# Performance work log

Hardware: AMD Instinct MI355X
Metric: run time of the kernel (lower is better)

Reference implementation:

```python
import jax, jax.numpy as jnp
import numpy as np

B, P, NOBJ = 16, 19248, 32
NUM_CLASSES = 81  # 80 foreground + background (code uses num_classes+1 w/o focal loss)
POS_TH, NEG_TH = 0.5, 0.4
VAR0, VAR1 = 0.1, 0.2  # standard SSD encode variances
NEGPOS_RATIO = 3


def setup_inputs() -> dict:
    key = jax.random.key(0)
    k1, k2, k3, k4, k5 = jax.random.split(key, 5)
    loc_data = jax.random.normal(k1, (B, P, 4), jnp.float32)
    conf_data = jax.random.normal(k2, (B, P, NUM_CLASSES), jnp.float32)
    # priors in (cx, cy, w, h), normalized coords
    pc = jax.random.uniform(k3, (P, 2), jnp.float32, 0.05, 0.95)
    pw = jax.random.uniform(jax.random.fold_in(k3, 1), (P, 2), jnp.float32, 0.05, 0.4)
    priors = jnp.concatenate([pc, pw], -1)
    # gt boxes in point form (xmin, ymin, xmax, ymax)
    gc = jax.random.uniform(k4, (B, NOBJ, 2), jnp.float32, 0.2, 0.8)
    gw = jax.random.uniform(jax.random.fold_in(k4, 1), (B, NOBJ, 2), jnp.float32, 0.05, 0.3)
    gt_boxes = jnp.concatenate([gc - gw / 2, gc + gw / 2], -1)
    gt_labels = jax.random.randint(k5, (B, NOBJ), 0, NUM_CLASSES - 1)  # 0..79
    return {"loc_data": loc_data, "conf_data": conf_data, "priors": priors,
            "gt_boxes": gt_boxes, "gt_labels": gt_labels}


def _point_form(p):
    # (cx,cy,w,h) -> (xmin,ymin,xmax,ymax)
    return jnp.concatenate([p[..., :2] - p[..., 2:] / 2, p[..., :2] + p[..., 2:] / 2], -1)


def _jaccard(a, b):
    # a: [N,4], b: [P,4] point form -> IoU [N,P]
    lt = jnp.maximum(a[:, None, :2], b[None, :, :2])
    rb = jnp.minimum(a[:, None, 2:], b[None, :, 2:])
    wh = jnp.clip(rb - lt, 0.0)
    inter = wh[..., 0] * wh[..., 1]
    area_a = (a[:, 2] - a[:, 0]) * (a[:, 3] - a[:, 1])
    area_b = (b[:, 2] - b[:, 0]) * (b[:, 3] - b[:, 1])
    return inter / (area_a[:, None] + area_b[None, :] - inter)


def _match_one(gt, labels, priors_pf, priors):
    # SSD match: per-prior best gt + force each gt's best prior to be positive
    ov = _jaccard(gt, priors_pf)                 # [N,P]
    best_prior_idx = jnp.argmax(ov, axis=1)      # [N]
    best_truth_ov = jnp.max(ov, axis=0)          # [P]
    best_truth_idx = jnp.argmax(ov, axis=0)      # [P]
    best_truth_ov = best_truth_ov.at[best_prior_idx].set(2.0)
    best_truth_idx = best_truth_idx.at[best_prior_idx].set(jnp.arange(gt.shape[0]))
    matched = gt[best_truth_idx]                 # [P,4] point form
    conf = labels[best_truth_idx] + 1
    conf = jnp.where(best_truth_ov < POS_TH, -1, conf)   # neutral band
    conf = jnp.where(best_truth_ov < NEG_TH, 0, conf)    # background
    # encode offsets with variances
    m_cxcy = (matched[:, :2] + matched[:, 2:]) / 2
    m_wh = matched[:, 2:] - matched[:, :2]
    g_cxcy = (m_cxcy - priors[:, :2]) / (VAR0 * priors[:, 2:])
    g_wh = jnp.log(m_wh / priors[:, 2:]) / VAR1
    return jnp.concatenate([g_cxcy, g_wh], -1), conf


def reference(loc_data, conf_data, priors, gt_boxes, gt_labels):
    priors_pf = _point_form(priors)
    loc_t, conf_t = jax.vmap(lambda g, l: _match_one(g, l, priors_pf, priors))(gt_boxes, gt_labels)
    loc_t = jax.lax.stop_gradient(loc_t)
    pos = conf_t > 0                                   # [B,P]
    n_pos = pos.sum(axis=1)                            # [B]
    N = jnp.maximum(pos.sum(), 1).astype(loc_data.dtype)
    # localization: smooth L1 over positives
    d = loc_data - loc_t
    ad = jnp.abs(d)
    sl1 = jnp.where(ad < 1.0, 0.5 * d * d, ad - 0.5)
    loss_l = jnp.sum(sl1 * pos[..., None])
    # confidence: hard negative mining at 3:1
    logp = jax.nn.log_softmax(conf_data, axis=-1)      # [B,P,C]
    ct = jnp.maximum(conf_t, 0)
    nll = -jnp.take_along_axis(logp, ct[..., None], axis=-1)[..., 0]  # [B,P]
    mine = jnp.where(pos | (conf_t < 0), 0.0, nll)     # exclude pos & neutral from mining
    rank = jnp.argsort(jnp.argsort(-mine, axis=1), axis=1)
    num_neg = jnp.minimum(NEGPOS_RATIO * n_pos, P - 1)
    neg = (rank < num_neg[:, None]) & (conf_t == 0)
    loss_c = jnp.sum(nll * (pos | neg))
    return jnp.stack([loss_l, loss_c]) / N
```

## Files before the change

### kernel.cpp

```cpp
#include <hip/hip_runtime.h>
#include <cstdint>
#include <cstddef>

#define BB 16
#define PP 19248
#define NOBJ 32
#define NCLS 81
#define POS_TH 0.5f
#define NEG_TH 0.4f
#define VAR0 0.1f
#define VAR1 0.2f
#define NEGPOS 3

#define MTB 256
#define NMB ((PP + MTB - 1) / MTB)
#define MAINB 1024
#define ROWS_PB 64
#define NSLOT ((PP + ROWS_PB - 1) / ROWS_PB)
#define NSLOTW (NSLOT * 16)
#define ST 1024

#define MCH 8
#define CHLEN (PP / MCH)
#define MJOBS (BB * NOBJ * MCH)
#define MBLK (MJOBS / 4)

#define HSHIFT 19
#define HSIZE 8192
#define HPT (HSIZE / ST)
#define CAP HSIZE

__global__ __launch_bounds__(MTB) void k_match(const float* __restrict__ priors,
                                               const float* __restrict__ gt_boxes,
                                               unsigned long long* __restrict__ gkey) {
    const int wid = threadIdx.x >> 6, lane = threadIdx.x & 63;
    const int job = blockIdx.x * 4 + wid;
    const int b = job >> 8;
    const int n = (job >> 3) & 31;
    const int c = job & 7;

    const float4 g = ((const float4*)gt_boxes)[b * NOBJ + n];
    float garea;
    {
#pragma clang fp contract(off)
        garea = (g.z - g.x) * (g.w - g.y);
    }

    unsigned long long bestkey = 0ull;
    const int pbeg = c * CHLEN;
    const int pend = pbeg + CHLEN;
    for (int p = pbeg + lane; p < pend; p += 64) {
        float4 pr = ((const float4*)priors)[p];
        float iou;
        {
#pragma clang fp contract(off)
            float hw = pr.z / 2.0f, hh = pr.w / 2.0f;
            float px1 = pr.x - hw, py1 = pr.y - hh, px2 = pr.x + hw, py2 = pr.y + hh;
            float parea = (px2 - px1) * (py2 - py1);
            float ix1 = fmaxf(g.x, px1), iy1 = fmaxf(g.y, py1);
            float ix2 = fminf(g.z, px2), iy2 = fminf(g.w, py2);
            float iw = fmaxf(ix2 - ix1, 0.0f), ih = fmaxf(iy2 - iy1, 0.0f);
            float inter = iw * ih;
            iou = inter / (garea + parea - inter);
        }
        unsigned long long key = (((unsigned long long)__float_as_uint(iou)) << 32) |
                                 (unsigned long long)(0xFFFFFFFFu - (unsigned)p);
        if (key > bestkey) bestkey = key;
    }
#pragma unroll
    for (int m = 1; m < 64; m <<= 1) {
        unsigned long long o = __shfl_xor(bestkey, m, 64);
        if (o > bestkey) bestkey = o;
    }
    if (lane == 0) atomicMax(&gkey[b * NOBJ + n], bestkey);
}

__global__ __launch_bounds__(MTB) void k_prior(const float* __restrict__ priors,
                                               const float* __restrict__ gt_boxes,
                                               int* __restrict__ bp) {
    const int b = blockIdx.y;
    const int p = blockIdx.x * MTB + threadIdx.x;
    __shared__ float4 sg[NOBJ];
    if (threadIdx.x < NOBJ) sg[threadIdx.x] = ((const float4*)gt_boxes)[b * NOBJ + threadIdx.x];
    __syncthreads();
    if (p >= PP) return;

    float4 pr = ((const float4*)priors)[p];
    float px1, py1, px2, py2, parea;
    {
#pragma clang fp contract(off)
        float hw = pr.z / 2.0f, hh = pr.w / 2.0f;
        px1 = pr.x - hw; py1 = pr.y - hh; px2 = pr.x + hw; py2 = pr.y + hh;
        parea = (px2 - px1) * (py2 - py1);
    }

    float best = -1.0f;
    int bn = 0;
#pragma unroll 4
    for (int n = 0; n < NOBJ; ++n) {
        float4 g = sg[n];
        float iou;
        {
#pragma clang fp contract(off)
            float ix1 = fmaxf(g.x, px1), iy1 = fmaxf(g.y, py1);
            float ix2 = fminf(g.z, px2), iy2 = fminf(g.w, py2);
            float iw = fmaxf(ix2 - ix1, 0.0f), ih = fmaxf(iy2 - iy1, 0.0f);
            float inter = iw * ih;
            float garea = (g.z - g.x) * (g.w - g.y);
            iou = inter / (garea + parea - inter);
        }
        if (iou > best) { best = iou; bn = n; }
    }
    int cls = 2;
    if (best < POS_TH) cls = 1;
    if (best < NEG_TH) cls = 0;
    bp[(size_t)b * PP + p] = (bn << 2) | cls;
}

__device__ __forceinline__ float sl1(float d) {
    float ad = fabsf(d);
    return ad < 1.0f ? 0.5f * d * d : ad - 0.5f;
}

__global__ __launch_bounds__(MAINB) void k_main(const float* __restrict__ loc_data,
                                                const float* __restrict__ conf_data,
                                                const float* __restrict__ priors,
                                                const float* __restrict__ gt_boxes,
                                                const int* __restrict__ gt_labels,
                                                const int* __restrict__ bp,
                                                const unsigned long long* __restrict__ gkey,
                                                float* __restrict__ mine,
                                                float* __restrict__ p_ll,
                                                float* __restrict__ p_lc,
                                                int* __restrict__ p_np) {
    const int b = blockIdx.y;
    const int t = threadIdx.x;
    const int wid = t >> 6;
    const int lane = t & 63;
    const int g = lane >> 4;
    const int j = lane & 15;
    const int rbase = blockIdx.x * ROWS_PB + wid * 4;
    const int r = rbase + g;
    const bool valid = r < PP;
    const int slot = blockIdx.x * 16 + wid;

    unsigned pst = 0xFFFFFFFFu;
    int labreg = 0;
    if (lane < NOBJ) {
        pst = 0xFFFFFFFFu - (unsigned)(gkey[b * NOBJ + lane] & 0xFFFFFFFFull);
        labreg = gt_labels[b * NOBJ + lane];
    }

    const float* rowp = conf_data + ((size_t)b * PP + r) * NCLS;
    float c0 = 0.f, c1 = 0.f, c2 = 0.f, c3 = 0.f, c4 = 0.f, c80 = 0.f;
    int packed = 0;
    if (valid) {
        c0 = rowp[j];
        c1 = rowp[j + 16];
        c2 = rowp[j + 32];
        c3 = rowp[j + 48];
        c4 = rowp[j + 64];
        if (j == 0) c80 = rowp[80];
        packed = bp[(size_t)b * PP + r];
    }

    float s = __expf(c0) + __expf(c1) + __expf(c2) + __expf(c3) + __expf(c4);
    if (j == 0) s += __expf(c80);
    s += __shfl_xor(s, 1, 64);
    s += __shfl_xor(s, 2, 64);
    s += __shfl_xor(s, 4, 64);
    s += __shfl_xor(s, 8, 64);
    const float lse = __logf(s);

    unsigned long long b0 = __ballot(pst == (unsigned)(rbase + 0));
    unsigned long long b1 = __ballot(pst == (unsigned)(rbase + 1));
    unsigned long long b2 = __ballot(pst == (unsigned)(rbase + 2));
    unsigned long long b3 = __ballot(pst == (unsigned)(rbase + 3));
    unsigned long long mball = (g == 0) ? b0 : (g == 1) ? b1 : (g == 2) ? b2 : b3;

    int ti = packed >> 2;
    int cls = packed & 3;
    if (mball) { ti = 63 - __builtin_clzll(mball); cls = 2; }

    const int lab = __shfl(labreg, ti, 64);
    int conf_c = (cls == 2) ? (lab + 1) : ((cls == 1) ? -1 : 0);

    const float row0 = __shfl(c0, lane & 48, 64);
    const float nll0 = lse - row0;

    float my_ll = 0.0f, my_lc = 0.0f;
    int my_pos = 0;

    if (valid && j == 0) {
        mine[(size_t)b * PP + r] = (conf_c == 0) ? nll0 : 0.0f;
        if (conf_c > 0) {
            my_pos = 1;
            my_lc = lse - rowp[conf_c];
            float4 gbox = ((const float4*)gt_boxes)[b * NOBJ + ti];
            float4 pr = ((const float4*)priors)[r];
            float mcx = (gbox.x + gbox.z) / 2.0f, mcy = (gbox.y + gbox.w) / 2.0f;
            float mw = gbox.z - gbox.x, mh = gbox.w - gbox.y;
            float t0 = (mcx - pr.x) / (VAR0 * pr.z);
            float t1 = (mcy - pr.y) / (VAR0 * pr.w);
            float t2 = logf(mw / pr.z) / VAR1;
            float t3 = logf(mh / pr.w) / VAR1;
            float4 ld = ((const float4*)loc_data)[(size_t)b * PP + r];
            my_ll = sl1(ld.x - t0) + sl1(ld.y - t1) + sl1(ld.z - t2) + sl1(ld.w - t3);
        }
    }

    if (__ballot(my_pos != 0) == 0ull) {
        if (lane == 0) {
            p_ll[b * NSLOTW + slot] = 0.0f;
            p_lc[b * NSLOTW + slot] = 0.0f;
            p_np[b * NSLOTW + slot] = 0;
        }
    } else {
        for (int off = 32; off > 0; off >>= 1) {
            my_ll += __shfl_down(my_ll, off, 64);
            my_lc += __shfl_down(my_lc, off, 64);
            my_pos += __shfl_down(my_pos, off, 64);
        }
        if (lane == 0) {
            p_ll[b * NSLOTW + slot] = my_ll;
            p_lc[b * NSLOTW + slot] = my_lc;
            p_np[b * NSLOTW + slot] = my_pos;
        }
    }
}

__global__ __launch_bounds__(ST) void k_select(const float* __restrict__ mine,
                                               const float* __restrict__ p_ll,
                                               const float* __restrict__ p_lc,
                                               const int* __restrict__ p_np,
                                               float* __restrict__ acc,
                                               int* __restrict__ acc_np,
                                               unsigned* __restrict__ done,
                                               float* __restrict__ out) {
    const int b = blockIdx.x;
    const int tid = threadIdx.x;
    const int wid = tid >> 6, lane = tid & 63;
    constexpr int NW = ST / 64;

    __shared__ unsigned hist[HSIZE];
    __shared__ unsigned s_tsum[ST];
    __shared__ unsigned s_wsum[NW];
    __shared__ float rll[NW], rlc[NW];
    __shared__ int rnp[NW];
    __shared__ float rs1[NW], rs2[NW];
    __shared__ unsigned rc2[NW];
    __shared__ float s_ll, s_lc, s_neg;
    __shared__ int s_np, s_B, s_G1;
    __shared__ unsigned s_cntB, s_cnt, s_prefix;
    __shared__ int s_rem;
    __shared__ unsigned h16[16];
    __shared__ unsigned swh[NW * 16];
    __shared__ unsigned stot[16];

    float ll = 0.0f, lc = 0.0f;
    int np = 0;
    for (int i = tid; i < NSLOTW; i += ST) {
        ll += p_ll[b * NSLOTW + i];
        lc += p_lc[b * NSLOTW + i];
        np += p_np[b * NSLOTW + i];
    }
    for (int off = 32; off > 0; off >>= 1) {
        ll += __shfl_down(ll, off, 64);
        lc += __shfl_down(lc, off, 64);
        np += __shfl_down(np, off, 64);
    }
    if (lane == 0) { rll[wid] = ll; rlc[wid] = lc; rnp[wid] = np; }
    __syncthreads();
    if (tid == 0) {
        float a = 0.0f, c = 0.0f;
        int n = 0;
        for (int w = 0; w < NW; ++w) { a += rll[w]; c += rlc[w]; n += rnp[w]; }
        s_ll = a; s_lc = c; s_np = n;
        s_neg = 0.0f;
    }
    __syncthreads();
    const int np_b = s_np;
    const int k = min(NEGPOS * np_b, PP - 1);

    const float* mv = mine + (size_t)b * PP;
    const float4* mv4 = (const float4*)mv;
    constexpr int PP4 = PP / 4;

    if (k > 0) {
        for (int i = tid; i < HSIZE; i += ST) hist[i] = 0u;
        __syncthreads();
        for (int i = tid; i < PP4; i += ST) {
            float4 v = mv4[i];
            atomicAdd(&hist[__float_as_uint(v.x) >> HSHIFT], 1u);
            atomicAdd(&hist[__float_as_uint(v.y) >> HSHIFT], 1u);
            atomicAdd(&hist[__float_as_uint(v.z) >> HSHIFT], 1u);
            atomicAdd(&hist[__float_as_uint(v.w) >> HSHIFT], 1u);
        }
        __syncthreads();

        unsigned tsum = 0;
        const int hb = tid * HPT;
#pragma unroll
        for (int v = 0; v < HPT; ++v) tsum += hist[hb + v];
        s_tsum[tid] = tsum;
        unsigned wsum = tsum;
        for (int off = 32; off > 0; off >>= 1) wsum += __shfl_down(wsum, off, 64);
        if (lane == 0) s_wsum[wid] = wsum;
        __syncthreads();
        if (tid == 0) {
            unsigned cum = 0;
            int w = NW - 1;
            for (; w > 0; --w) {
                if (cum + s_wsum[w] >= (unsigned)k) break;
                cum += s_wsum[w];
            }
            int t = (w + 1) * 64 - 1;
            for (; t > w * 64; --t) {
                if (cum + s_tsum[t] >= (unsigned)k) break;
                cum += s_tsum[t];
            }
            int bin = t * HPT + HPT - 1;
            for (; bin > t * HPT; --bin) {
                if (cum + hist[bin] >= (unsigned)k) break;
                cum += hist[bin];
            }
            s_B = bin;
            s_G1 = (int)cum;
            s_cntB = hist[bin];
            s_cnt = 0u;
        }
        __syncthreads();
        const int B = s_B;
        const int r = k - s_G1;
        const unsigned cntB = s_cntB;
        const unsigned bin_lo = (unsigned)B << HSHIFT;
        const unsigned hi_base = (unsigned)(B + 1) << HSHIFT;
        unsigned* cbuf = hist;

        if (cntB <= CAP) {
            float S1 = 0.0f;
            for (int i = tid; i < PP4; i += ST) {
                float4 v = mv4[i];
                unsigned bx = __float_as_uint(v.x);
                unsigned by = __float_as_uint(v.y);
                unsigned bz = __float_as_uint(v.z);
                unsigned bw = __float_as_uint(v.w);
                if (bx >= hi_base) S1 += v.x;
                else if (bx >= bin_lo) cbuf[atomicAdd(&s_cnt, 1u)] = bx;
                if (by >= hi_base) S1 += v.y;
                else if (by >= bin_lo) cbuf[atomicAdd(&s_cnt, 1u)] = by;
                if (bz >= hi_base) S1 += v.z;
                else if (bz >= bin_lo) cbuf[atomicAdd(&s_cnt, 1u)] = bz;
                if (bw >= hi_base) S1 += v.w;
                else if (bw >= bin_lo) cbuf[atomicAdd(&s_cnt, 1u)] = bw;
            }
            for (int off = 32; off > 0; off >>= 1) S1 += __shfl_down(S1, off, 64);
            if (lane == 0) rs1[wid] = S1;
            __syncthreads();

            if (tid == 0) { s_prefix = bin_lo; s_rem = r; }
            __syncthreads();
            for (int pass = 0; pass < 5; ++pass) {
                const int shift = (pass < 4) ? (15 - 4 * pass) : 0;
                const int width = (pass < 4) ? 4 : 3;
                const int nb = 1 << width;
                const unsigned hm = 0xFFFFFFFFu << (shift + width);
                if (tid < 16) h16[tid] = 0u;
                __syncthreads();
                const unsigned prefix = s_prefix;
                for (unsigned i = tid; i < cntB; i += ST) {
                    unsigned bits = cbuf[i];
                    if ((bits & hm) == prefix)
                        atomicAdd(&h16[(bits >> shift) & (nb - 1)], 1u);
                }
                __syncthreads();
                if (tid == 0) {
                    int rem = s_rem;
                    unsigned cum = 0;
                    int chosen = 0;
                    for (int v = nb - 1; v >= 0; --v) {
                        unsigned c = h16[v];
                        if (cum + c >= (unsigned)rem) { chosen = v; s_rem = rem - (int)cum; break; }
                        cum += c;
                    }
                    s_prefix = prefix | ((unsigned)chosen << shift);
                }
                __syncthreads();
            }
            const unsigned T = s_prefix;

            float S2 = 0.0f;
            unsigned c2 = 0;
            for (unsigned i = tid; i < cntB; i += ST) {
                unsigned bits = cbuf[i];
                if (bits > T) { S2 += __uint_as_float(bits); c2++; }
            }
            for (int off = 32; off > 0; off >>= 1) {
                S2 += __shfl_down(S2, off, 64);
                c2 += __shfl_down(c2, off, 64);
            }
            if (lane == 0) { rs2[wid] = S2; rc2[wid] = c2; }
            __syncthreads();
            if (tid == 0) {
                float S1t = 0.0f, S2t = 0.0f;
                unsigned c2t = 0;
                for (int w = 0; w < NW; ++w) { S1t += rs1[w]; S2t += rs2[w]; c2t += rc2[w]; }
                s_neg = S1t + S2t + (float)(r - (int)c2t) * __uint_as_float(T);
            }
            __syncthreads();
        } else {
            if (tid == 0) { s_prefix = 0u; s_rem = k; }
            __syncthreads();
            for (int pass = 0; pass < 8; ++pass) {
                const int shift = 28 - 4 * pass;
                const unsigned hm = (pass == 0) ? 0u : (0xFFFFFFFFu << (shift + 4));
                const unsigned prefix = s_prefix;
                unsigned cnt[16];
#pragma unroll
                for (int v = 0; v < 16; ++v) cnt[v] = 0u;
                for (int i = tid; i < PP; i += ST) {
                    unsigned bits = __float_as_uint(mv[i]);
                    unsigned key = ((bits & hm) == prefix) ? ((bits >> shift) & 15u) : 16u;
                    if (__any(key != 16u)) {
#pragma unroll
                        for (int v = 0; v < 16; ++v)
                            cnt[v] += (unsigned)__popcll(__ballot(key == (unsigned)v));
                    }
                }
                if (lane == 0) {
#pragma unroll
                    for (int v = 0; v < 16; ++v) swh[wid * 16 + v] = cnt[v];
                }
                __syncthreads();
                if (tid < 16) {
                    unsigned tt = 0;
#pragma unroll
                    for (int w = 0; w < NW; ++w) tt += swh[w * 16 + tid];
                    stot[tid] = tt;
                }
                __syncthreads();
                if (tid == 0) {
                    int rem = s_rem;
                    unsigned cum = 0;
                    int chosen = 0;
                    for (int v = 15; v >= 0; --v) {
                        unsigned c = stot[v];
                        if (cum + c >= (unsigned)rem) { chosen = v; s_rem = rem - (int)cum; break; }
                        cum += c;
                    }
                    s_prefix = prefix | ((unsigned)chosen << shift);
                }
                __syncthreads();
            }
            const unsigned T = s_prefix;
            float sum = 0.0f;
            unsigned cnt = 0;
            for (int i = tid; i < PP; i += ST) {
                float v = mv[i];
                if (__float_as_uint(v) > T) { sum += v; cnt++; }
            }
            for (int off = 32; off > 0; off >>= 1) {
                sum += __shfl_down(sum, off, 64);
                cnt += __shfl_down(cnt, off, 64);
            }
            if (lane == 0) { rs2[wid] = sum; rc2[wid] = cnt; }
            __syncthreads();
            if (tid == 0) {
                float S = 0.0f;
                int G = 0;
                for (int w = 0; w < NW; ++w) { S += rs2[w]; G += (int)rc2[w]; }
                s_neg = S + (float)(k - G) * __uint_as_float(T);
            }
            __syncthreads();
        }
    }

    if (tid == 0) {
        atomicAdd(&acc[0], s_ll);
        atomicAdd(&acc[1], s_lc + s_neg);
        atomicAdd(acc_np, np_b);
        __threadfence();
        unsigned prev = atomicAdd(done, 1u);
        if (prev == BB - 1) {
            int tp = atomicAdd(acc_np, 0);
            float N = (float)max(tp, 1);
            float a0 = atomicAdd(&acc[0], 0.0f);
            float a1 = atomicAdd(&acc[1], 0.0f);
            out[0] = a0 / N;
            out[1] = a1 / N;
        }
    }
}

extern "C" void kernel_launch(void* const* d_in, const int* in_sizes, int n_in,
                              void* d_out, int out_size, void* d_ws, size_t ws_size,
                              hipStream_t stream) {
    const float* loc    = (const float*)d_in[0];
    const float* conf   = (const float*)d_in[1];
    const float* priors = (const float*)d_in[2];
    const float* gt     = (const float*)d_in[3];
    const int*   labels = (const int*)d_in[4];
    float* out = (float*)d_out;

    char* ws = (char*)d_ws;
    const size_t SZ_BP = (size_t)BB * PP * 4;
    const size_t SZ_SLOT = (size_t)BB * NSLOTW * 4;
    unsigned long long* gkey = (unsigned long long*)ws;
    float*    acc    = (float*)   (ws + 4096);
    int*      acc_np = (int*)     (ws + 4104);
    unsigned* done   = (unsigned*)(ws + 4108);
    int*   bp   = (int*)  (ws + 4224);
    float* mine = (float*)(ws + 4224 + SZ_BP);
    float* p_ll = (float*)(ws + 4224 + 2 * SZ_BP);
    float* p_lc = (float*)(ws + 4224 + 2 * SZ_BP + SZ_SLOT);
    int*   p_np = (int*)  (ws + 4224 + 2 * SZ_BP + 2 * SZ_SLOT);

    (void)hipMemsetAsync(ws, 0, 4224, stream);

    k_match<<<MBLK, MTB, 0, stream>>>(priors, gt, gkey);

    dim3 pg(NMB, BB);
    k_prior<<<pg, MTB, 0, stream>>>(priors, gt, bp);

    dim3 kg(NSLOT, BB);
    k_main<<<kg, MAINB, 0, stream>>>(loc, conf, priors, gt, labels, bp, gkey,
                                     mine, p_ll, p_lc, p_np);

    k_select<<<BB, ST, 0, stream>>>(mine, p_ll, p_lc, p_np, acc, acc_np, done, out);
}
```

Before: 213.6 us.

## Apply forced matches in separate kernel and pack labels into prior map

Moves forced best-prior assignment out of k_main into a small k_force kernel that atomically overwrites the per-prior packed word, and has k_prior store the final label code directly. k_main no longer loads gkey/labels, runs four ballots, or shuffles the label per row. It also now processes 8 rows per wave with 8 lanes each (10 loads per lane), which halves the number of k_main blocks. The cost is an extra kernel launch plus serialized atomics. The packed-word encoding must preserve the priority of forced matches, with the largest n winning ties.

```diff
diff --git a/kernel.cpp b/kernel.cpp
--- a/kernel.cpp
+++ b/kernel.cpp
@@ -15,7 +15,7 @@
 #define MTB 256
 #define NMB ((PP + MTB - 1) / MTB)
 #define MAINB 1024
-#define ROWS_PB 64
+#define ROWS_PB 128
 #define NSLOT ((PP + ROWS_PB - 1) / ROWS_PB)
 #define NSLOTW (NSLOT * 16)
 #define ST 1024
@@ -77,11 +77,16 @@
 
 __global__ __launch_bounds__(MTB) void k_prior(const float* __restrict__ priors,
                                                const float* __restrict__ gt_boxes,
-                                               int* __restrict__ bp) {
+                                               const int* __restrict__ gt_labels,
+                                               unsigned* __restrict__ bp) {
     const int b = blockIdx.y;
     const int p = blockIdx.x * MTB + threadIdx.x;
     __shared__ float4 sg[NOBJ];
-    if (threadIdx.x < NOBJ) sg[threadIdx.x] = ((const float4*)gt_boxes)[b * NOBJ + threadIdx.x];
+    __shared__ int slab[NOBJ];
+    if (threadIdx.x < NOBJ) {
+        sg[threadIdx.x] = ((const float4*)gt_boxes)[b * NOBJ + threadIdx.x];
+        slab[threadIdx.x] = gt_labels[b * NOBJ + threadIdx.x];
+    }
     __syncthreads();
     if (p >= PP) return;
 
@@ -111,10 +116,23 @@
         }
         if (iou > best) { best = iou; bn = n; }
     }
-    int cls = 2;
-    if (best < POS_TH) cls = 1;
-    if (best < NEG_TH) cls = 0;
-    bp[(size_t)b * PP + p] = (bn << 2) | cls;
+    unsigned cc;
+    if (best < NEG_TH) cc = 1u;
+    else if (best < POS_TH) cc = 0u;
+    else cc = (unsigned)(slab[bn] + 2);
+    bp[(size_t)b * PP + p] = ((unsigned)bn << 8) | cc;
+}
+
+__global__ __launch_bounds__(512) void k_force(const int* __restrict__ gt_labels,
+                                               const unsigned long long* __restrict__ gkey,
+                                               unsigned* __restrict__ bp) {
+    const int i = threadIdx.x;
+    const int b = i >> 5, n = i & 31;
+    unsigned long long key = gkey[b * NOBJ + n];
+    unsigned pstar = 0xFFFFFFFFu - (unsigned)(key & 0xFFFFFFFFull);
+    int lab = gt_labels[b * NOBJ + n];
+    unsigned val = 0x80000000u | ((unsigned)n << 8) | (unsigned)(lab + 2);
+    atomicMax(&bp[(size_t)b * PP + pstar], val);
 }
 
 __device__ __forceinline__ float sl1(float d) {
@@ -126,9 +144,7 @@
                                                 const float* __restrict__ conf_data,
                                                 const float* __restrict__ priors,
                                                 const float* __restrict__ gt_boxes,
-                                                const int* __restrict__ gt_labels,
-                                                const int* __restrict__ bp,
-                                                const unsigned long long* __restrict__ gkey,
+                                                const unsigned* __restrict__ bp,
                                                 float* __restrict__ mine,
                                                 float* __restrict__ p_ll,
                                                 float* __restrict__ p_lc,
@@ -137,65 +153,46 @@
     const int t = threadIdx.x;
     const int wid = t >> 6;
     const int lane = t & 63;
-    const int g = lane >> 4;
-    const int j = lane & 15;
-    const int rbase = blockIdx.x * ROWS_PB + wid * 4;
+    const int g = lane >> 3;
+    const int j = lane & 7;
+    const int rbase = blockIdx.x * ROWS_PB + wid * 8;
     const int r = rbase + g;
     const bool valid = r < PP;
     const int slot = blockIdx.x * 16 + wid;
 
-    unsigned pst = 0xFFFFFFFFu;
-    int labreg = 0;
-    if (lane < NOBJ) {
-        pst = 0xFFFFFFFFu - (unsigned)(gkey[b * NOBJ + lane] & 0xFFFFFFFFull);
-        labreg = gt_labels[b * NOBJ + lane];
-    }
-
     const float* rowp = conf_data + ((size_t)b * PP + r) * NCLS;
-    float c0 = 0.f, c1 = 0.f, c2 = 0.f, c3 = 0.f, c4 = 0.f, c80 = 0.f;
-    int packed = 0;
+    float c[10];
+#pragma unroll
+    for (int i = 0; i < 10; ++i) c[i] = 0.0f;
+    float c80 = 0.0f;
+    unsigned w = 1u;
     if (valid) {
-        c0 = rowp[j];
-        c1 = rowp[j + 16];
-        c2 = rowp[j + 32];
-        c3 = rowp[j + 48];
-        c4 = rowp[j + 64];
+#pragma unroll
+        for (int i = 0; i < 10; ++i) c[i] = rowp[j + 8 * i];
         if (j == 0) c80 = rowp[80];
-        packed = bp[(size_t)b * PP + r];
-    }
-
-    float s = __expf(c0) + __expf(c1) + __expf(c2) + __expf(c3) + __expf(c4);
+        w = bp[(size_t)b * PP + r];
+    }
+
+    float s = 0.0f;
+#pragma unroll
+    for (int i = 0; i < 10; ++i) s += __expf(c[i]);
     if (j == 0) s += __expf(c80);
     s += __shfl_xor(s, 1, 64);
     s += __shfl_xor(s, 2, 64);
     s += __shfl_xor(s, 4, 64);
-    s += __shfl_xor(s, 8, 64);
     const float lse = __logf(s);
 
-    unsigned long long b0 = __ballot(pst == (unsigned)(rbase + 0));
-    unsigned long long b1 = __ballot(pst == (unsigned)(rbase + 1));
-    unsigned long long b2 = __ballot(pst == (unsigned)(rbase + 2));
-    unsigned long long b3 = __ballot(pst == (unsigned)(rbase + 3));
-    unsigned long long mball = (g == 0) ? b0 : (g == 1) ? b1 : (g == 2) ? b2 : b3;
-
-    int ti = packed >> 2;
-    int cls = packed & 3;
-    if (mball) { ti = 63 - __builtin_clzll(mball); cls = 2; }
-
-    const int lab = __shfl(labreg, ti, 64);
-    int conf_c = (cls == 2) ? (lab + 1) : ((cls == 1) ? -1 : 0);
-
-    const float row0 = __shfl(c0, lane & 48, 64);
-    const float nll0 = lse - row0;
+    const int cc = (int)(w & 0xFFu);
 
     float my_ll = 0.0f, my_lc = 0.0f;
     int my_pos = 0;
 
     if (valid && j == 0) {
-        mine[(size_t)b * PP + r] = (conf_c == 0) ? nll0 : 0.0f;
-        if (conf_c > 0) {
+        mine[(size_t)b * PP + r] = (cc == 1) ? (lse - c[0]) : 0.0f;
+        if (cc >= 2) {
             my_pos = 1;
-            my_lc = lse - rowp[conf_c];
+            my_lc = lse - rowp[cc - 1];
+            const int ti = (int)((w >> 8) & 63u);
             float4 gbox = ((const float4*)gt_boxes)[b * NOBJ + ti];
             float4 pr = ((const float4*)priors)[r];
             float mcx = (gbox.x + gbox.z) / 2.0f, mcy = (gbox.y + gbox.w) / 2.0f;
@@ -509,7 +506,7 @@
     float*    acc    = (float*)   (ws + 4096);
     int*      acc_np = (int*)     (ws + 4104);
     unsigned* done   = (unsigned*)(ws + 4108);
-    int*   bp   = (int*)  (ws + 4224);
+    unsigned* bp  = (unsigned*)(ws + 4224);
     float* mine = (float*)(ws + 4224 + SZ_BP);
     float* p_ll = (float*)(ws + 4224 + 2 * SZ_BP);
     float* p_lc = (float*)(ws + 4224 + 2 * SZ_BP + SZ_SLOT);
@@ -520,10 +517,12 @@
     k_match<<<MBLK, MTB, 0, stream>>>(priors, gt, gkey);
 
     dim3 pg(NMB, BB);
-    k_prior<<<pg, MTB, 0, stream>>>(priors, gt, bp);
+    k_prior<<<pg, MTB, 0, stream>>>(priors, gt, labels, bp);
+
+    k_force<<<1, 512, 0, stream>>>(labels, gkey, bp);
 
     dim3 kg(NSLOT, BB);
-    k_main<<<kg, MAINB, 0, stream>>>(loc, conf, priors, gt, labels, bp, gkey,
+    k_main<<<kg, MAINB, 0, stream>>>(loc, conf, priors, gt, bp,
                                      mine, p_ll, p_lc, p_np);
 
     k_select<<<BB, ST, 0, stream>>>(mine, p_ll, p_lc, p_np, acc, acc_np, done, out);
```

Result: no change. 210.7 us (median of 2 runs) (-1.3%).
